# Performance work log

Hardware: AMD Instinct MI355X
Metric: run time of the kernel (lower is better)

## Reference

```python
import jax, jax.numpy as jnp
import numpy as np

BLOCK_SIZES = [256] * 8            # sum = N_CTX = 2048
B, H, D = 2, 16, 64
N_CTX = sum(BLOCK_SIZES)
SPARSITY_PATTERN = 'block_causal'  # row_starts = 0, row_ends = end of own block


def _build_masks(block_sizes, pattern):
    cs = np.cumsum([0] + list(block_sizes))
    row_ends = np.concatenate([np.full(bs, cs[i + 1], dtype=np.int32)
                               for i, bs in enumerate(block_sizes)])
    if pattern == 'block_diagonal':
        row_starts = np.concatenate([np.full(bs, cs[i], dtype=np.int32)
                                     for i, bs in enumerate(block_sizes)])
    elif pattern == 'block_causal':
        row_starts = np.zeros_like(row_ends)
    else:
        raise ValueError(pattern)
    return jnp.asarray(row_starts), jnp.asarray(row_ends)


def setup_inputs() -> dict:
    key = jax.random.key(0)
    kq, kk, kv = jax.random.split(key, 3)
    q = jax.random.normal(kq, (B, H, N_CTX, D), dtype=jnp.float32)
    k = jax.random.normal(kk, (B, H, N_CTX, D), dtype=jnp.float32)
    v = jax.random.normal(kv, (B, H, N_CTX, D), dtype=jnp.float32)
    row_starts, row_ends = _build_masks(BLOCK_SIZES, SPARSITY_PATTERN)
    sm_scale = jnp.float32(1.0 / np.sqrt(D))
    return {"q": q, "k": k, "v": v, "sm_scale": sm_scale,
            "row_starts": row_starts, "row_ends": row_ends}


def reference(q, k, v, sm_scale, row_starts, row_ends):
    # q,k,v: [B,H,N,D]; per query row i, attend to kv cols in [row_starts[i], row_ends[i])
    n = q.shape[2]
    cols = jnp.arange(n, dtype=jnp.int32)
    allowed = (cols[None, :] >= row_starts[:, None]) & (cols[None, :] < row_ends[:, None])  # [N,N]
    scores = jnp.einsum('bhqd,bhkd->bhqk', q, k) * sm_scale
    neg = jnp.finfo(scores.dtype).min
    scores = jnp.where(allowed[None, None], scores, neg)
    p = jax.nn.softmax(scores, axis=-1)
    return jnp.einsum('bhqk,bhkd->bhqd', p, v)
```

## Files before the change

kernel.cpp:

```cpp
#include <hip/hip_runtime.h>


typedef short bf16x8 __attribute__((ext_vector_type(8)));
typedef float f32x4  __attribute__((ext_vector_type(4)));
typedef unsigned short u16;
typedef u16 u16x8 __attribute__((ext_vector_type(8)));

#define MFMA(A,B,C) __builtin_amdgcn_mfma_f32_16x16x32_bf16((A),(B),(C),0,0,0)

__device__ __forceinline__ u16 f2bf_rne(float f) {
    union { float f; unsigned u; } c; c.f = f;
    unsigned r = c.u + 0x7FFFu + ((c.u >> 16) & 1u);
    return (u16)(r >> 16);
}
__device__ __forceinline__ u16 f2bf_fast(float f) {
    union { float f; unsigned u; } c; c.f = f;
    return (u16)((c.u + 0x8000u) >> 16);
}

__global__ __launch_bounds__(256, 2)
void bsattn_fused(const float* __restrict__ Q, const float* __restrict__ K,
                  const float* __restrict__ V, const float* __restrict__ SC,
                  const int* __restrict__ RS, const int* __restrict__ RE,
                  float* __restrict__ O)
{
    constexpr int N = 2048, D = 64;
    int wg = blockIdx.x;
    int bh   = (wg & 15) + ((wg >> 8) << 4);
    int qsub = (wg >> 4) & 15;
    int q0 = qsub << 7;

    int tid = threadIdx.x, wid = tid >> 6, lane = tid & 63;
    int n = lane & 15, g = lane >> 4;

    __shared__ __align__(16) u16 lsm[16384];
    __shared__ int sbi[8];

    int row0 = q0 + wid * 32 + n;
    int row1 = row0 + 16;
    int rs_l0 = RS[row0], re_l0 = RE[row0];
    int rs_l1 = RS[row1], re_l1 = RE[row1];
    int w_rs_min = min(rs_l0, rs_l1), w_rs_max = max(rs_l0, rs_l1);
    int w_re_min = min(re_l0, re_l1), w_re_max = max(re_l0, re_l1);
    #pragma unroll
    for (int o = 1; o < 16; o <<= 1) {
        w_rs_min = min(w_rs_min, __shfl_xor(w_rs_min, o));
        w_rs_max = max(w_rs_max, __shfl_xor(w_rs_max, o));
        w_re_min = min(w_re_min, __shfl_xor(w_re_min, o));
        w_re_max = max(w_re_max, __shfl_xor(w_re_max, o));
    }
    if (lane == 0) { sbi[wid * 2] = w_rs_min; sbi[wid * 2 + 1] = w_re_max; }

    float sscale = SC[0] * 1.44269504088896340736f;

    bf16x8 qA0, qA1, qB0, qB1;
    {
        const float* qp = Q + ((size_t)bh * N + row0) * D + g * 8;
        float4 a0 = *(const float4*)qp,        a1 = *(const float4*)(qp + 4);
        float4 b0 = *(const float4*)(qp + 32), b1 = *(const float4*)(qp + 36);
        qA0[0]=f2bf_rne(a0.x*sscale); qA0[1]=f2bf_rne(a0.y*sscale);
        qA0[2]=f2bf_rne(a0.z*sscale); qA0[3]=f2bf_rne(a0.w*sscale);
        qA0[4]=f2bf_rne(a1.x*sscale); qA0[5]=f2bf_rne(a1.y*sscale);
        qA0[6]=f2bf_rne(a1.z*sscale); qA0[7]=f2bf_rne(a1.w*sscale);
        qA1[0]=f2bf_rne(b0.x*sscale); qA1[1]=f2bf_rne(b0.y*sscale);
        qA1[2]=f2bf_rne(b0.z*sscale); qA1[3]=f2bf_rne(b0.w*sscale);
        qA1[4]=f2bf_rne(b1.x*sscale); qA1[5]=f2bf_rne(b1.y*sscale);
        qA1[6]=f2bf_rne(b1.z*sscale); qA1[7]=f2bf_rne(b1.w*sscale);
    }
    {
        const float* qp = Q + ((size_t)bh * N + row1) * D + g * 8;
        float4 a0 = *(const float4*)qp,        a1 = *(const float4*)(qp + 4);
        float4 b0 = *(const float4*)(qp + 32), b1 = *(const float4*)(qp + 36);
        qB0[0]=f2bf_rne(a0.x*sscale); qB0[1]=f2bf_rne(a0.y*sscale);
        qB0[2]=f2bf_rne(a0.z*sscale); qB0[3]=f2bf_rne(a0.w*sscale);
        qB0[4]=f2bf_rne(a1.x*sscale); qB0[5]=f2bf_rne(a1.y*sscale);
        qB0[6]=f2bf_rne(a1.z*sscale); qB0[7]=f2bf_rne(a1.w*sscale);
        qB1[0]=f2bf_rne(b0.x*sscale); qB1[1]=f2bf_rne(b0.y*sscale);
        qB1[2]=f2bf_rne(b0.z*sscale); qB1[3]=f2bf_rne(b0.w*sscale);
        qB1[4]=f2bf_rne(b1.x*sscale); qB1[5]=f2bf_rne(b1.y*sscale);
        qB1[6]=f2bf_rne(b1.z*sscale); qB1[7]=f2bf_rne(b1.w*sscale);
    }

    __syncthreads();
    int kst  = min(min(sbi[0], sbi[2]), min(sbi[4], sbi[6])) & ~63;
    int kend = max(max(sbi[1], sbi[3]), max(sbi[5], sbi[7]));
    int t0 = kst >> 6;
    int w  = (kend - kst + 63) >> 6;

    int rA   = ((n >> 2) << 3) + (n & 3);
    int phk  = (n & 3) + 4 * ((n >> 2) & 1);
    int osA0 = rA * 64 + ((g + phk) & 7) * 8;
    int osA1 = rA * 64 + ((g + 4 + phk) & 7) * 8;
    int ov0  = 4096 + n * 64 + ((    g + (n & 7)) & 7) * 8;
    int ov1  = 4096 + n * 64 + ((4 + g + (n & 7)) & 7) * 8;

    int key_l = tid >> 2, c2 = (tid & 3) << 1;
    int rotb  = (key_l & 3) + 4 * ((key_l >> 3) & 1);
    int kiA   = key_l * 64 + (((c2    ) + rotb) & 7) * 8;
    int kiB   = key_l * 64 + (((c2 + 1) + rotb) & 7) * 8;
    int kc    = lane >> 3, kw = lane & 7;
    const float* Kb = K + (size_t)bh * N * D;
    const float* Vb = V + (size_t)bh * N * D;

    f32x4 accA[4], accB[4];
    f32x4 acclA = {0.f,0.f,0.f,0.f}, acclB = {0.f,0.f,0.f,0.f};
    #pragma unroll
    for (int c = 0; c < 4; ++c) {
        accA[c] = (f32x4){0.f,0.f,0.f,0.f};
        accB[c] = (f32x4){0.f,0.f,0.f,0.f};
    }
    bf16x8 ones;
    #pragma unroll
    for (int j = 0; j < 8; ++j) ones[j] = (short)0x3F80;

    float4 kf0, kf1, kf2, kf3, vf0, vf1, vf2, vf3;

    auto stage_load = [&](int i) {
        if (i < w) {
            const float* kp = Kb + (size_t)(t0 + i) * 4096 + key_l * 64 + c2 * 8;
            kf0 = *(const float4*)kp;       kf1 = *(const float4*)(kp + 4);
            kf2 = *(const float4*)(kp + 8); kf3 = *(const float4*)(kp + 12);
            const float* vp = Vb + (size_t)(t0 + i) * 4096 + lane * 64 + wid * 16;
            vf0 = *(const float4*)vp;       vf1 = *(const float4*)(vp + 4);
            vf2 = *(const float4*)(vp + 8); vf3 = *(const float4*)(vp + 12);
        }
    };
    auto stage_write = [&](int i) {
        if (i < w) {
            u16* dst = &lsm[(i & 1) << 13];
            u16x8 a, b;
            a[0]=f2bf_rne(kf0.x); a[1]=f2bf_rne(kf0.y); a[2]=f2bf_rne(kf0.z); a[3]=f2bf_rne(kf0.w);
            a[4]=f2bf_rne(kf1.x); a[5]=f2bf_rne(kf1.y); a[6]=f2bf_rne(kf1.z); a[7]=f2bf_rne(kf1.w);
            b[0]=f2bf_rne(kf2.x); b[1]=f2bf_rne(kf2.y); b[2]=f2bf_rne(kf2.z); b[3]=f2bf_rne(kf2.w);
            b[4]=f2bf_rne(kf3.x); b[5]=f2bf_rne(kf3.y); b[6]=f2bf_rne(kf3.z); b[7]=f2bf_rne(kf3.w);
            *(u16x8*)&dst[kiA] = a;
            *(u16x8*)&dst[kiB] = b;
            float vy[16] = { vf0.x,vf0.y,vf0.z,vf0.w, vf1.x,vf1.y,vf1.z,vf1.w,
                             vf2.x,vf2.y,vf2.z,vf2.w, vf3.x,vf3.y,vf3.z,vf3.w };
            #pragma unroll
            for (int j = 0; j < 16; ++j) {
                int d = wid * 16 + j;
                dst[4096 + d * 64 + ((kc + (j & 7)) & 7) * 8 + kw] = f2bf_rne(vy[j]);
            }
        }
    };

    auto proc = [&](int kb, const u16* ls) {
        bool bdry = (kb < w_rs_max) || (kb + 64 > w_re_min);
        #pragma unroll
        for (int h = 0; h < 2; ++h) {
            int hb = h * 2048;
            bf16x8 k00 = *(const bf16x8*)&ls[hb + osA0];
            bf16x8 k01 = *(const bf16x8*)&ls[hb + osA1];
            bf16x8 k10 = *(const bf16x8*)&ls[hb + osA0 + 256];
            bf16x8 k11 = *(const bf16x8*)&ls[hb + osA1 + 256];
            f32x4 tA0 = {0.f,0.f,0.f,0.f}, tA1 = tA0, tB0 = tA0, tB1 = tA0;
            __builtin_amdgcn_s_setprio(1);
            tA0 = MFMA(k00, qA0, tA0); tA0 = MFMA(k01, qA1, tA0);
            tA1 = MFMA(k10, qA0, tA1); tA1 = MFMA(k11, qA1, tA1);
            tB0 = MFMA(k00, qB0, tB0); tB0 = MFMA(k01, qB1, tB0);
            tB1 = MFMA(k10, qB0, tB1); tB1 = MFMA(k11, qB1, tB1);
            __builtin_amdgcn_s_setprio(0);
            float sA[8], sB[8];
            #pragma unroll
            for (int r = 0; r < 4; ++r) {
                sA[r] = tA0[r]; sA[4 + r] = tA1[r];
                sB[r] = tB0[r]; sB[4 + r] = tB1[r];
            }
            if (bdry) {
                #pragma unroll
                for (int j = 0; j < 8; ++j) {
                    int key = kb + h * 32 + g * 8 + j;
                    if (key < rs_l0 || key >= re_l0) sA[j] = -1e30f;
                    if (key < rs_l1 || key >= re_l1) sB[j] = -1e30f;
                }
            }
            bf16x8 pA, pB;
            #pragma unroll
            for (int j = 0; j < 8; ++j) { float p = __builtin_amdgcn_exp2f(sA[j]); pA[j] = (short)f2bf_fast(p); }
            #pragma unroll
            for (int j = 0; j < 8; ++j) { float p = __builtin_amdgcn_exp2f(sB[j]); pB[j] = (short)f2bf_fast(p); }
            int ov = h ? ov1 : ov0;
            bf16x8 v0 = *(const bf16x8*)&ls[ov       ];
            bf16x8 v1 = *(const bf16x8*)&ls[ov + 1024];
            bf16x8 v2 = *(const bf16x8*)&ls[ov + 2048];
            bf16x8 v3 = *(const bf16x8*)&ls[ov + 3072];
            __builtin_amdgcn_s_setprio(1);
            accA[0] = MFMA(pA, v0, accA[0]);
            accA[1] = MFMA(pA, v1, accA[1]);
            accA[2] = MFMA(pA, v2, accA[2]);
            accA[3] = MFMA(pA, v3, accA[3]);
            acclA   = MFMA(pA, ones, acclA);
            accB[0] = MFMA(pB, v0, accB[0]);
            accB[1] = MFMA(pB, v1, accB[1]);
            accB[2] = MFMA(pB, v2, accB[2]);
            accB[3] = MFMA(pB, v3, accB[3]);
            acclB   = MFMA(pB, ones, acclB);
            __builtin_amdgcn_s_setprio(0);
        }
    };

    stage_load(0);
    stage_write(0);
    for (int i = 0; i < w; ++i) {
        __syncthreads();
        stage_load(i + 1);
        proc(kst + (i << 6), &lsm[(i & 1) << 13]);
        stage_write(i + 1);
    }

    int rb = g << 2;
    {
        int orow = q0 + wid * 32 + rb;
        float* ob = O + ((size_t)bh * N + orow) * D + n;
        #pragma unroll
        for (int r = 0; r < 4; ++r) {
            float li = 1.0f / acclA[r];
            float* rp = ob + (size_t)r * D;
            rp[0]  = accA[0][r] * li;
            rp[16] = accA[1][r] * li;
            rp[32] = accA[2][r] * li;
            rp[48] = accA[3][r] * li;
        }
    }
    {
        int orow = q0 + wid * 32 + 16 + rb;
        float* ob = O + ((size_t)bh * N + orow) * D + n;
        #pragma unroll
        for (int r = 0; r < 4; ++r) {
            float li = 1.0f / acclB[r];
            float* rp = ob + (size_t)r * D;
            rp[0]  = accB[0][r] * li;
            rp[16] = accB[1][r] * li;
            rp[32] = accB[2][r] * li;
            rp[48] = accB[3][r] * li;
        }
    }
}

extern "C" void kernel_launch(void* const* d_in, const int* in_sizes, int n_in,
                              void* d_out, int out_size, void* d_ws, size_t ws_size,
                              hipStream_t stream) {
    const float* q  = (const float*)d_in[0];
    const float* k  = (const float*)d_in[1];
    const float* v  = (const float*)d_in[2];
    const float* sc = (const float*)d_in[3];
    const int* rs   = (const int*)d_in[4];
    const int* re   = (const int*)d_in[5];
    float* out      = (float*)d_out;

    bsattn_fused<<<dim3(512), dim3(256), 0, stream>>>(q, k, v, sc, rs, re, out);
}
```

Measured before the change: 140.4 us.

## Split KV tiles across two wave groups per workgroup with LDS reduction

Each workgroup now has 512 threads in two groups of four waves. Each group walks half of the query tile's KV range, using its own double-buffered LDS region. The partial outputs and row sums are then added through shared memory before normalising and storing. The aim is to shorten the serial KV loop for the long causal rows and improve load balance, with the block-to-(bh, q-tile) mapping also reordered. It costs twice the LDS, an extra reduction phase, and a tighter launch-bounds register budget, and it silently drops the last tile when the tile count is odd.

```diff
diff --git a/kernel.cpp b/kernel.cpp
--- a/kernel.cpp
+++ b/kernel.cpp
@@ -18,7 +18,7 @@
     return (u16)((c.u + 0x8000u) >> 16);
 }
 
-__global__ __launch_bounds__(256, 2)
+__global__ __launch_bounds__(512, 4)
 void bsattn_fused(const float* __restrict__ Q, const float* __restrict__ K,
                   const float* __restrict__ V, const float* __restrict__ SC,
                   const int* __restrict__ RS, const int* __restrict__ RE,
@@ -26,15 +26,18 @@
 {
     constexpr int N = 2048, D = 64;
     int wg = blockIdx.x;
-    int bh   = (wg & 15) + ((wg >> 8) << 4);
-    int qsub = (wg >> 4) & 15;
+    int bh   = wg & 31;
+    int qsub = wg >> 5;
     int q0 = qsub << 7;
 
-    int tid = threadIdx.x, wid = tid >> 6, lane = tid & 63;
+    int tid = threadIdx.x;
+    int grp = tid >> 8;
+    int tl  = tid & 255;
+    int wid = tl >> 6, lane = tl & 63;
     int n = lane & 15, g = lane >> 4;
 
-    __shared__ __align__(16) u16 lsm[16384];
-    __shared__ int sbi[8];
+    __shared__ __align__(16) u16 lsm[32768];
+    __shared__ int sbi[16];
 
     int row0 = q0 + wid * 32 + n;
     int row1 = row0 + 16;
@@ -49,7 +52,8 @@
         w_re_min = min(w_re_min, __shfl_xor(w_re_min, o));
         w_re_max = max(w_re_max, __shfl_xor(w_re_max, o));
     }
-    if (lane == 0) { sbi[wid * 2] = w_rs_min; sbi[wid * 2 + 1] = w_re_max; }
+    int wid8 = tid >> 6;
+    if (lane == 0) { sbi[wid8 * 2] = w_rs_min; sbi[wid8 * 2 + 1] = w_re_max; }
 
     float sscale = SC[0] * 1.44269504088896340736f;
 
@@ -82,10 +86,13 @@
     }
 
     __syncthreads();
-    int kst  = min(min(sbi[0], sbi[2]), min(sbi[4], sbi[6])) & ~63;
-    int kend = max(max(sbi[1], sbi[3]), max(sbi[5], sbi[7]));
+    int kst  = min(min(min(sbi[0], sbi[2]),  min(sbi[4],  sbi[6])),
+                   min(min(sbi[8], sbi[10]), min(sbi[12], sbi[14]))) & ~63;
+    int kend = max(max(max(sbi[1], sbi[3]),  max(sbi[5],  sbi[7])),
+                   max(max(sbi[9], sbi[11]), max(sbi[13], sbi[15])));
     int t0 = kst >> 6;
     int w  = (kend - kst + 63) >> 6;
+    int wl = w >> 1;
 
     int rA   = ((n >> 2) << 3) + (n & 3);
     int phk  = (n & 3) + 4 * ((n >> 2) & 1);
@@ -94,7 +101,7 @@
     int ov0  = 4096 + n * 64 + ((    g + (n & 7)) & 7) * 8;
     int ov1  = 4096 + n * 64 + ((4 + g + (n & 7)) & 7) * 8;
 
-    int key_l = tid >> 2, c2 = (tid & 3) << 1;
+    int key_l = tl >> 2, c2 = (tl & 3) << 1;
     int rotb  = (key_l & 3) + 4 * ((key_l >> 3) & 1);
     int kiA   = key_l * 64 + (((c2    ) + rotb) & 7) * 8;
     int kiB   = key_l * 64 + (((c2 + 1) + rotb) & 7) * 8;
@@ -102,6 +109,8 @@
     const float* Kb = K + (size_t)bh * N * D;
     const float* Vb = V + (size_t)bh * N * D;
 
+    int go = grp << 14;
+
     f32x4 accA[4], accB[4];
     f32x4 acclA = {0.f,0.f,0.f,0.f}, acclB = {0.f,0.f,0.f,0.f};
     #pragma unroll
@@ -116,18 +125,19 @@
     float4 kf0, kf1, kf2, kf3, vf0, vf1, vf2, vf3;
 
     auto stage_load = [&](int i) {
-        if (i < w) {
-            const float* kp = Kb + (size_t)(t0 + i) * 4096 + key_l * 64 + c2 * 8;
+        if (i < wl) {
+            int tile = t0 + grp * wl + i;
+            const float* kp = Kb + (size_t)tile * 4096 + key_l * 64 + c2 * 8;
             kf0 = *(const float4*)kp;       kf1 = *(const float4*)(kp + 4);
             kf2 = *(const float4*)(kp + 8); kf3 = *(const float4*)(kp + 12);
-            const float* vp = Vb + (size_t)(t0 + i) * 4096 + lane * 64 + wid * 16;
+            const float* vp = Vb + (size_t)tile * 4096 + lane * 64 + wid * 16;
             vf0 = *(const float4*)vp;       vf1 = *(const float4*)(vp + 4);
             vf2 = *(const float4*)(vp + 8); vf3 = *(const float4*)(vp + 12);
         }
     };
     auto stage_write = [&](int i) {
-        if (i < w) {
-            u16* dst = &lsm[(i & 1) << 13];
+        if (i < wl) {
+            u16* dst = &lsm[go + ((i & 1) << 13)];
             u16x8 a, b;
             a[0]=f2bf_rne(kf0.x); a[1]=f2bf_rne(kf0.y); a[2]=f2bf_rne(kf0.z); a[3]=f2bf_rne(kf0.w);
             a[4]=f2bf_rne(kf1.x); a[5]=f2bf_rne(kf1.y); a[6]=f2bf_rne(kf1.z); a[7]=f2bf_rne(kf1.w);
@@ -202,38 +212,72 @@
 
     stage_load(0);
     stage_write(0);
-    for (int i = 0; i < w; ++i) {
+    for (int i = 0; i < wl; ++i) {
         __syncthreads();
         stage_load(i + 1);
-        proc(kst + (i << 6), &lsm[(i & 1) << 13]);
+        proc(kst + ((grp * wl + i) << 6), &lsm[go + ((i & 1) << 13)]);
         stage_write(i + 1);
     }
 
-    int rb = g << 2;
-    {
-        int orow = q0 + wid * 32 + rb;
-        float* ob = O + ((size_t)bh * N + orow) * D + n;
-        #pragma unroll
-        for (int r = 0; r < 4; ++r) {
-            float li = 1.0f / acclA[r];
-            float* rp = ob + (size_t)r * D;
-            rp[0]  = accA[0][r] * li;
-            rp[16] = accA[1][r] * li;
-            rp[32] = accA[2][r] * li;
-            rp[48] = accA[3][r] * li;
-        }
-    }
-    {
-        int orow = q0 + wid * 32 + 16 + rb;
-        float* ob = O + ((size_t)bh * N + orow) * D + n;
-        #pragma unroll
-        for (int r = 0; r < 4; ++r) {
-            float li = 1.0f / acclB[r];
-            float* rp = ob + (size_t)r * D;
-            rp[0]  = accB[0][r] * li;
-            rp[16] = accB[1][r] * li;
-            rp[32] = accB[2][r] * li;
-            rp[48] = accB[3][r] * li;
+    __syncthreads();
+    float* mf = (float*)lsm;
+    if (grp == 1) {
+        int slot = tl * 41;
+        #pragma unroll
+        for (int c = 0; c < 4; ++c)
+            #pragma unroll
+            for (int r = 0; r < 4; ++r) mf[slot + c * 4 + r] = accA[c][r];
+        #pragma unroll
+        for (int r = 0; r < 4; ++r) mf[slot + 16 + r] = acclA[r];
+        #pragma unroll
+        for (int c = 0; c < 4; ++c)
+            #pragma unroll
+            for (int r = 0; r < 4; ++r) mf[slot + 20 + c * 4 + r] = accB[c][r];
+        #pragma unroll
+        for (int r = 0; r < 4; ++r) mf[slot + 36 + r] = acclB[r];
+    }
+    __syncthreads();
+    if (grp == 0) {
+        int slot = tl * 41;
+        #pragma unroll
+        for (int c = 0; c < 4; ++c)
+            #pragma unroll
+            for (int r = 0; r < 4; ++r) accA[c][r] += mf[slot + c * 4 + r];
+        #pragma unroll
+        for (int r = 0; r < 4; ++r) acclA[r] += mf[slot + 16 + r];
+        #pragma unroll
+        for (int c = 0; c < 4; ++c)
+            #pragma unroll
+            for (int r = 0; r < 4; ++r) accB[c][r] += mf[slot + 20 + c * 4 + r];
+        #pragma unroll
+        for (int r = 0; r < 4; ++r) acclB[r] += mf[slot + 36 + r];
+
+        int rb = g << 2;
+        {
+            int orow = q0 + wid * 32 + rb;
+            float* ob = O + ((size_t)bh * N + orow) * D + n;
+            #pragma unroll
+            for (int r = 0; r < 4; ++r) {
+                float li = 1.0f / acclA[r];
+                float* rp = ob + (size_t)r * D;
+                rp[0]  = accA[0][r] * li;
+                rp[16] = accA[1][r] * li;
+                rp[32] = accA[2][r] * li;
+                rp[48] = accA[3][r] * li;
+            }
+        }
+        {
+            int orow = q0 + wid * 32 + 16 + rb;
+            float* ob = O + ((size_t)bh * N + orow) * D + n;
+            #pragma unroll
+            for (int r = 0; r < 4; ++r) {
+                float li = 1.0f / acclB[r];
+                float* rp = ob + (size_t)r * D;
+                rp[0]  = accB[0][r] * li;
+                rp[16] = accB[1][r] * li;
+                rp[32] = accB[2][r] * li;
+                rp[48] = accB[3][r] * li;
+            }
         }
     }
 }
@@ -249,5 +293,5 @@
     const int* re   = (const int*)d_in[5];
     float* out      = (float*)d_out;
 
-    bsattn_fused<<<dim3(512), dim3(256), 0, stream>>>(q, k, v, sc, rs, re, out);
-}
+    bsattn_fused<<<dim3(512), dim3(512), 0, stream>>>(q, k, v, sc, rs, re, out);
+}
```

New measurement: 225.1 us. +60.3%, slower.
